# Optimization experiments

Hardware: AMD Instinct MI355X
Metric: run time of the kernel (lower is better)

Reference implementation:

```python
import jax, jax.numpy as jnp
import numpy as np

DIM = 768
NUM_HEADS = 12
HEAD_DIM = DIM // NUM_HEADS
EPS = 1e-5


def setup_inputs() -> dict:
    key = jax.random.key(0)
    ks = jax.random.split(key, 9)
    s = 1.0 / np.sqrt(DIM)
    x = jax.random.normal(ks[0], (8, 1024, DIM), dtype=jnp.float32)
    Wq = jax.random.uniform(ks[1], (DIM, DIM), jnp.float32, -s, s)
    bq = jax.random.uniform(ks[2], (DIM,), jnp.float32, -s, s)
    Wk = jax.random.uniform(ks[3], (DIM, DIM), jnp.float32, -s, s)
    bk = jax.random.uniform(ks[4], (DIM,), jnp.float32, -s, s)
    Wv = jax.random.uniform(ks[5], (DIM, DIM), jnp.float32, -s, s)
    bv = jax.random.uniform(ks[6], (DIM,), jnp.float32, -s, s)
    Wo = jax.random.uniform(ks[7], (DIM, DIM), jnp.float32, -s, s)
    bo = jax.random.uniform(ks[8], (DIM,), jnp.float32, -s, s)
    ln_g = jnp.ones((DIM,), jnp.float32)
    ln_b = jnp.zeros((DIM,), jnp.float32)
    return {"x": x, "Wq": Wq, "bq": bq, "Wk": Wk, "bk": bk, "Wv": Wv,
            "bv": bv, "Wo": Wo, "bo": bo, "ln_g": ln_g, "ln_b": ln_b}


def _layernorm(h, g, b):
    mu = jnp.mean(h, axis=-1, keepdims=True)
    var = jnp.mean(jnp.square(h - mu), axis=-1, keepdims=True)
    return (h - mu) * jax.lax.rsqrt(var + EPS) * g + b


def reference(x, Wq, bq, Wk, bk, Wv, bv, Wo, bo, ln_g, ln_b):
    B, N, C = x.shape
    H, D = NUM_HEADS, HEAD_DIM
    scaling = D ** -0.5
    q = (x @ Wq.T + bq) * scaling          # [B,N,C]
    k = x @ Wk.T + bk
    v = x @ Wv.T + bv
    q = q.reshape(B, N, H, D).transpose(0, 2, 1, 3)  # [B,H,N,D]
    k = k.reshape(B, N, H, D).transpose(0, 2, 1, 3)
    v = v.reshape(B, N, H, D).transpose(0, 2, 1, 3)
    scores = jnp.einsum('bhnd,bhmd->bhnm', q, k)     # [B,H,N,N]
    probs = jax.nn.softmax(scores.astype(jnp.float32), axis=-1).astype(scores.dtype)
    attn = jnp.einsum('bhnm,bhmd->bhnd', probs, v)   # [B,H,N,D]
    attn = attn.transpose(0, 2, 1, 3).reshape(B, N, C)
    attn = _layernorm(attn, ln_g, ln_b)
    return attn @ Wo.T + bo
```

## Files before the change

kernel.cpp:

```cpp
#include <hip/hip_runtime.h>
#include <hip/hip_bf16.h>
#include <stdint.h>


using short8  = __attribute__((ext_vector_type(8))) short;
using short4v = __attribute__((ext_vector_type(4))) short;
using floatx4 = __attribute__((ext_vector_type(4))) float;

#define LOG2E 1.44269504088896340736f

typedef __attribute__((address_space(3))) uint32_t lds_u32;
typedef const __attribute__((address_space(1))) uint32_t glb_u32;
__device__ __forceinline__ void async_copy16(const void* g, void* l) {
  __builtin_amdgcn_global_load_lds((glb_u32*)g, (lds_u32*)l, 16, 0, 0);
}

__device__ __forceinline__ float b2f(int s) {
  return __builtin_bit_cast(float, (uint32_t)((uint16_t)s) << 16);
}
__device__ __forceinline__ short f2b(float f) {
  uint32_t u = __builtin_bit_cast(uint32_t, f);
  u += 0x7fffu + ((u >> 16) & 1u);
  return (short)(u >> 16);
}
__device__ __forceinline__ uint32_t pk2(float a, float b) {
#if defined(__has_builtin) && __has_builtin(__builtin_amdgcn_cvt_pk_bf16_f32)
  typedef __bf16 bf16x2 __attribute__((ext_vector_type(2)));
  return __builtin_bit_cast(uint32_t, __builtin_amdgcn_cvt_pk_bf16_f32(a, b));
#else
  return (uint32_t)(uint16_t)f2b(a) | ((uint32_t)(uint16_t)f2b(b) << 16);
#endif
}
__device__ __forceinline__ float fexp2(float x) {
#if defined(__has_builtin) && __has_builtin(__builtin_amdgcn_exp2f)
  return __builtin_amdgcn_exp2f(x);
#else
  return exp2f(x);
#endif
}
__device__ __forceinline__ float loadf(const void* p, int idx, bool f32) {
  return f32 ? ((const float*)p)[idx] : b2f(((const short*)p)[idx]);
}
__device__ __forceinline__ short8 load8f(const void* p, int idx) {
  const float* q = (const float*)p + idx;
  float4 x0 = *(const float4*)q, x1 = *(const float4*)(q + 4);
  short8 v = {f2b(x0.x), f2b(x0.y), f2b(x0.z), f2b(x0.w),
              f2b(x1.x), f2b(x1.y), f2b(x1.z), f2b(x1.w)};
  return v;
}

__global__ __launch_bounds__(256) void cvt1_k(
    const void* __restrict__ x, const void* __restrict__ wq,
    const void* __restrict__ wk, const void* __restrict__ wv,
    const void* __restrict__ bq, const void* __restrict__ bk,
    const void* __restrict__ bv, short* __restrict__ xb,
    short* __restrict__ wqkvb, short* __restrict__ bqkvb,
    const unsigned short* __restrict__ probe) {
  if (probe[0] == 0x3F80u) return;
  int idx = blockIdx.x * 256 + threadIdx.x;
  if (idx < 786432) { *(short8*)&xb[idx * 8] = load8f(x, idx * 8); return; }
  idx -= 786432;
  if (idx < 73728) { *(short8*)&wqkvb[idx * 8] = load8f(wq, idx * 8); return; }
  idx -= 73728;
  if (idx < 73728) { *(short8*)&wqkvb[589824 + idx * 8] = load8f(wk, idx * 8); return; }
  idx -= 73728;
  if (idx < 73728) { *(short8*)&wqkvb[1179648 + idx * 8] = load8f(wv, idx * 8); return; }
  idx -= 73728;
  if (idx < 96) { *(short8*)&bqkvb[idx * 8] = load8f(bq, idx * 8); return; }
  idx -= 96;
  if (idx < 96) { *(short8*)&bqkvb[768 + idx * 8] = load8f(bk, idx * 8); return; }
  idx -= 96;
  if (idx < 96) { *(short8*)&bqkvb[1536 + idx * 8] = load8f(bv, idx * 8); return; }
}

__device__ __forceinline__ void gemm_core(const short* __restrict__ Ab,
                                          const short* __restrict__ Bb,
                                          short (*sA)[4096], short (*sB)[4096],
                                          floatx4 (&acc)[4][4]) {
  const int t = threadIdx.x;
  const int w = t >> 6, l = t & 63;
  const int lrow = l & 15, quad = l >> 4;
  const int rw = (w >> 1) * 64, cw = (w & 1) * 64;
  const int ci0 = t, ci1 = 256 + t;
  const int row0 = ci0 >> 2, ch0 = (ci0 & 3) ^ ((ci0 >> 3) & 3);
  const int row1 = ci1 >> 2, ch1 = (ci1 & 3) ^ ((ci1 >> 3) & 3);
  const short* a0 = Ab + row0 * 768 + ch0 * 8;
  const short* b0 = Bb + row0 * 768 + ch0 * 8;
  const short* a1 = Ab + row1 * 768 + ch1 * 8;
  const short* b1 = Bb + row1 * 768 + ch1 * 8;
  const int ssel = (quad ^ ((lrow >> 1) & 3)) * 8;

#define STAGE(BUF, K0)                                      \
  async_copy16(a0 + (K0), (char*)sA[BUF] + ci0 * 16);       \
  async_copy16(b0 + (K0), (char*)sB[BUF] + ci0 * 16);       \
  async_copy16(a1 + (K0), (char*)sA[BUF] + ci1 * 16);       \
  async_copy16(b1 + (K0), (char*)sB[BUF] + ci1 * 16);

  STAGE(0, 0)
  STAGE(1, 32)

#pragma unroll
  for (int it = 0; it < 24; it++) {
    if (it < 23) { asm volatile("s_waitcnt vmcnt(4)" ::: "memory"); }
    else         { asm volatile("s_waitcnt vmcnt(0)" ::: "memory"); }
    __builtin_amdgcn_s_barrier();
    asm volatile("" ::: "memory");
    __builtin_amdgcn_sched_barrier(0);
    if (it + 2 < 24) {
      STAGE((it + 2) % 3, (it + 2) * 32)
    }
    const int cur = it % 3;
    short8 af[4], bf[4];
#pragma unroll
    for (int i = 0; i < 4; i++)
      af[i] = *(const short8*)&sA[cur][(rw + i * 16 + lrow) * 32 + ssel];
#pragma unroll
    for (int j = 0; j < 4; j++)
      bf[j] = *(const short8*)&sB[cur][(cw + j * 16 + lrow) * 32 + ssel];
#pragma unroll
    for (int i = 0; i < 4; i++)
#pragma unroll
      for (int j = 0; j < 4; j++)
        acc[i][j] =
            __builtin_amdgcn_mfma_f32_16x16x32_bf16(af[i], bf[j], acc[i][j], 0, 0, 0);
  }
#undef STAGE
}

__global__ __launch_bounds__(256, 3) void gemm_qkv_k(
    const void* __restrict__ x, const short* __restrict__ xb,
    const void* __restrict__ Wq, const void* __restrict__ Wk,
    const void* __restrict__ Wv, const short* __restrict__ wqkvb,
    const void* __restrict__ bq, const void* __restrict__ bk,
    const void* __restrict__ bv, const short* __restrict__ bqkvb,
    short* __restrict__ qo, short* __restrict__ ko, short* __restrict__ vo,
    const unsigned short* __restrict__ probe) {
  __shared__ __align__(16) short sA[3][4096];
  __shared__ __align__(16) short sB[3][4096];
  const bool f32 = (probe[0] != 0x3F80u);
  const int atile = blockIdx.x, btile = blockIdx.y;
  const int sel = btile / 6;

  const short* Ab = (f32 ? xb : (const short*)x) + atile * 98304;
  const short* Bb;
  const short* biasb;
  if (f32) {
    Bb = wqkvb + btile * 98304;
    biasb = bqkvb + sel * 768;
  } else {
    const void* Wsel = sel == 0 ? Wq : (sel == 1 ? Wk : Wv);
    Bb = (const short*)Wsel + (btile - sel * 6) * 98304;
    biasb = (const short*)(sel == 0 ? bq : (sel == 1 ? bk : bv));
  }

  floatx4 acc[4][4] = {};
  gemm_core(Ab, Bb, sA, sB, acc);

  const int t = threadIdx.x, w = t >> 6, l = t & 63;
  const int lrow = l & 15, quad = l >> 4;
  const int rw = (w >> 1) * 64, cw = (w & 1) * 64;
  const int nbase = (btile - sel * 6) * 128;
#pragma unroll
  for (int i = 0; i < 4; i++) {
    const int ra0 = atile * 128 + rw + i * 16 + quad * 4;
    const int bidx = ra0 >> 10, n_in_b = ra0 & 1023;
#pragma unroll
    for (int j = 0; j < 4; j++) {
      const int cb = nbase + cw + j * 16 + lrow;
      const float bias = b2f(biasb[cb]);
      const int hh = cb >> 6, dd = cb & 63;
      if (sel == 2) {
        short4v pv;
#pragma unroll
        for (int r = 0; r < 4; r++) pv[r] = f2b(acc[i][j][r] + bias);
        const int n64 = n_in_b & 63;
        const int pos = ((n64 >> 2) & 3) * 8 + (n64 & 32) + ((n64 >> 4) & 1) * 4;
        *(short4v*)&vo[(bidx * 12 + hh) * 65536 + dd * 1024 + (n_in_b & ~63) + pos] = pv;
      } else {
        const int base = (bidx * 12 + hh) * 65536 + dd;
        short* dst = sel == 0 ? qo : ko;
#pragma unroll
        for (int r = 0; r < 4; r++) {
          float v = acc[i][j][r] + bias;
          if (sel == 0) v *= (0.125f * LOG2E);
          dst[base + (n_in_b + r) * 64] = f2b(v);
        }
      }
    }
  }
}

__global__ __launch_bounds__(256, 3) void gemm_out_k(
    const short* __restrict__ ln, const void* __restrict__ Wo,
    const short* __restrict__ wob, const void* __restrict__ bo,
    const short* __restrict__ bob, void* __restrict__ out,
    const unsigned short* __restrict__ probe) {
  __shared__ __align__(16) short sA[3][4096];
  __shared__ __align__(16) short sB[3][4096];
  const bool f32 = (probe[0] != 0x3F80u);
  const int atile = blockIdx.x, btile = blockIdx.y;
  const short* Ab = ln + atile * 98304;
  const short* Bb = (f32 ? wob : (const short*)Wo) + btile * 98304;
  const short* biasb = f32 ? bob : (const short*)bo;

  floatx4 acc[4][4] = {};
  gemm_core(Ab, Bb, sA, sB, acc);

  const int t = threadIdx.x, w = t >> 6, l = t & 63;
  const int lrow = l & 15, quad = l >> 4;
  const int rw = (w >> 1) * 64, cw = (w & 1) * 64;
#pragma unroll
  for (int i = 0; i < 4; i++) {
    const int ra0 = atile * 128 + rw + i * 16 + quad * 4;
#pragma unroll
    for (int j = 0; j < 4; j++) {
      const int cb = btile * 128 + cw + j * 16 + lrow;
      const float bias = b2f(biasb[cb]);
#pragma unroll
      for (int r = 0; r < 4; r++) {
        float v = acc[i][j][r] + bias;
        if (f32) ((float*)out)[(ra0 + r) * 768 + cb] = v;
        else     ((short*)out)[(ra0 + r) * 768 + cb] = f2b(v);
      }
    }
  }
}

__global__ __launch_bounds__(256, 5) void attn_k(const short* __restrict__ q,
                                                 const short* __restrict__ k,
                                                 const short* __restrict__ vt,
                                                 short* __restrict__ o) {
  __shared__ __align__(16) short sMem[2][8192];

  const int t = threadIdx.x, w = t >> 6, l = t & 63;
  const int lrow = l & 15, quad = l >> 4;
  const int bh = blockIdx.x, qt = blockIdx.y;
  const int b = bh / 12, h = bh % 12;
  const short* qb = q + bh * 65536 + qt * 4096;
  const short* kb = k + bh * 65536;
  const short* vb = vt + bh * 65536;

  const int srow = t >> 3, sgc = (t & 7) ^ (srow & 7);
  const short* kst = kb + srow * 64 + sgc * 8;
  const short* vst = vb + srow * 1024 + sgc * 8;

  const int swz0 = (quad ^ (lrow & 7)) * 16;
  const int swz1 = ((4 + quad) ^ (lrow & 7)) * 16;
  const char* s0 = (const char*)&sMem[0][0];
  const char* kp0 = s0 + lrow * 128 + swz0;
  const char* kp1 = s0 + lrow * 128 + swz1;
  const char* vp0 = s0 + 8192 + lrow * 128 + swz0;
  const char* vp1 = s0 + 8192 + lrow * 128 + swz1;

#pragma unroll
  for (int i = 0; i < 2; i++) {
    const int ci = i * 256 + t;
    const int row = ci >> 3, gc = (ci & 7) ^ (row & 7);
    async_copy16(qb + row * 64 + gc * 8, (char*)sMem[1] + ci * 16);
  }
  async_copy16(kst, (char*)sMem[0] + t * 16);
  async_copy16(kst + 2048, (char*)sMem[0] + 4096 + t * 16);
  async_copy16(vst, (char*)sMem[0] + 8192 + t * 16);
  async_copy16(vst + 32768, (char*)sMem[0] + 12288 + t * 16);
  __syncthreads();

  short8 qf[2];
  const int qr = w * 16 + lrow;
#pragma unroll
  for (int dc = 0; dc < 2; dc++)
    qf[dc] = *(const short8*)&sMem[1][qr * 64 + ((dc * 4 + quad) ^ (qr & 7)) * 8];
  __syncthreads();

  const short one_b = (short)0x3F80;
  const short8 ones8 = {one_b, one_b, one_b, one_b, one_b, one_b, one_b, one_b};
  floatx4 l_acc = {};
  floatx4 o_acc[4] = {};

#define ATTN_BODY(CUR, IT)                                                     \
  {                                                                            \
    if ((IT) < 15) {                                                           \
      const int nxt = (CUR) ^ 1;                                               \
      const short* ksrc = kst + ((IT) + 1) * 4096;                             \
      const short* vsrc = vst + ((IT) + 1) * 64;                               \
      async_copy16(ksrc, (char*)sMem[nxt] + t * 16);                           \
      async_copy16(ksrc + 2048, (char*)sMem[nxt] + 4096 + t * 16);             \
      async_copy16(vsrc, (char*)sMem[nxt] + 8192 + t * 16);                    \
      async_copy16(vsrc + 32768, (char*)sMem[nxt] + 12288 + t * 16);           \
    }                                                                          \
    short4v pf[4];                                                             \
    _Pragma("unroll")                                                          \
    for (int g = 0; g < 4; g++) {                                              \
      short8 kf0 = *(const short8*)(kp0 + (CUR) * 16384 + g * 2048);           \
      short8 kf1 = *(const short8*)(kp1 + (CUR) * 16384 + g * 2048);           \
      floatx4 st = {};                                                         \
      st = __builtin_amdgcn_mfma_f32_16x16x32_bf16(kf0, qf[0], st, 0, 0, 0);   \
      st = __builtin_amdgcn_mfma_f32_16x16x32_bf16(kf1, qf[1], st, 0, 0, 0);   \
      uint2 pp = {pk2(fexp2(st[0]), fexp2(st[1])),                             \
                  pk2(fexp2(st[2]), fexp2(st[3]))};                            \
      pf[g] = __builtin_bit_cast(short4v, pp);                                 \
    }                                                                          \
    const short8 pa0 =                                                         \
        __builtin_shufflevector(pf[0], pf[1], 0, 1, 2, 3, 4, 5, 6, 7);         \
    const short8 pa1 =                                                         \
        __builtin_shufflevector(pf[2], pf[3], 0, 1, 2, 3, 4, 5, 6, 7);         \
    l_acc = __builtin_amdgcn_mfma_f32_16x16x32_bf16(pa0, ones8, l_acc, 0, 0, 0); \
    l_acc = __builtin_amdgcn_mfma_f32_16x16x32_bf16(pa1, ones8, l_acc, 0, 0, 0); \
    _Pragma("unroll")                                                          \
    for (int j2 = 0; j2 < 4; j2++) {                                           \
      short8 vv0 = *(const short8*)(vp0 + (CUR) * 16384 + j2 * 2048);          \
      short8 vv1 = *(const short8*)(vp1 + (CUR) * 16384 + j2 * 2048);          \
      o_acc[j2] =                                                              \
          __builtin_amdgcn_mfma_f32_16x16x32_bf16(pa0, vv0, o_acc[j2], 0, 0, 0); \
      o_acc[j2] =                                                              \
          __builtin_amdgcn_mfma_f32_16x16x32_bf16(pa1, vv1, o_acc[j2], 0, 0, 0); \
    }                                                                          \
    __syncthreads();                                                           \
  }

  for (int it2 = 0; it2 < 8; it2++) {
    ATTN_BODY(0, it2 * 2)
    ATTN_BODY(1, it2 * 2 + 1)
  }
#undef ATTN_BODY

  float inv_l[4];
#pragma unroll
  for (int r = 0; r < 4; r++) inv_l[r] = 1.0f / l_acc[r];
  const int n0 = qt * 64 + w * 16 + quad * 4;
#pragma unroll
  for (int j2 = 0; j2 < 4; j2++) {
    const int d = j2 * 16 + lrow;
#pragma unroll
    for (int r = 0; r < 4; r++)
      o[(b * 1024 + n0 + r) * 768 + h * 64 + d] = f2b(o_acc[j2][r] * inv_l[r]);
  }
}

__global__ __launch_bounds__(256) void lncvt_k(const short* __restrict__ in,
                                               const void* __restrict__ g,
                                               const void* __restrict__ be,
                                               short* __restrict__ out,
                                               const void* __restrict__ wo,
                                               const void* __restrict__ bo,
                                               short* __restrict__ wob,
                                               short* __restrict__ bob,
                                               const unsigned short* __restrict__ probe) {
  const bool f32 = (probe[0] != 0x3F80u);
  if (blockIdx.x >= 2048) {
    if (!f32) return;
    int idx = (blockIdx.x - 2048) * 256 + threadIdx.x;
    if (idx < 73728) { *(short8*)&wob[idx * 8] = load8f(wo, idx * 8); return; }
    idx -= 73728;
    if (idx < 96) { *(short8*)&bob[idx * 8] = load8f(bo, idx * 8); }
    return;
  }
  const int w = threadIdx.x >> 6, l = threadIdx.x & 63;
  const int row = blockIdx.x * 4 + w;
  const short* rp = in + row * 768;
  float v[12];
  float s = 0.f, ss = 0.f;
#pragma unroll
  for (int c = 0; c < 3; c++) {
    ushort4 u = *(const ushort4*)&rp[(c * 64 + l) * 4];
    float f0 = b2f(u.x), f1 = b2f(u.y), f2 = b2f(u.z), f3 = b2f(u.w);
    v[c * 4 + 0] = f0; v[c * 4 + 1] = f1; v[c * 4 + 2] = f2; v[c * 4 + 3] = f3;
    s += (f0 + f1) + (f2 + f3);
    ss += (f0 * f0 + f1 * f1) + (f2 * f2 + f3 * f3);
  }
#pragma unroll
  for (int msk = 1; msk < 64; msk <<= 1) {
    s += __shfl_xor(s, msk);
    ss += __shfl_xor(ss, msk);
  }
  const float mu = s * (1.f / 768.f);
  const float rstd = rsqrtf(ss * (1.f / 768.f) - mu * mu + 1e-5f);
  short* op = out + row * 768;
#pragma unroll
  for (int c = 0; c < 3; c++) {
    const int base = (c * 64 + l) * 4;
    ushort4 r;
    r.x = (unsigned short)(unsigned)f2b((v[c * 4 + 0] - mu) * rstd * loadf(g, base + 0, f32) + loadf(be, base + 0, f32));
    r.y = (unsigned short)(unsigned)f2b((v[c * 4 + 1] - mu) * rstd * loadf(g, base + 1, f32) + loadf(be, base + 1, f32));
    r.z = (unsigned short)(unsigned)f2b((v[c * 4 + 2] - mu) * rstd * loadf(g, base + 2, f32) + loadf(be, base + 2, f32));
    r.w = (unsigned short)(unsigned)f2b((v[c * 4 + 3] - mu) * rstd * loadf(g, base + 3, f32) + loadf(be, base + 3, f32));
    *(ushort4*)&op[base] = r;
  }
}

extern "C" void kernel_launch(void* const* d_in, const int* in_sizes, int n_in,
                              void* d_out, int out_size, void* d_ws, size_t ws_size,
                              hipStream_t stream) {
  const void* x    = d_in[0];
  const void* Wq   = d_in[1];
  const void* bq   = d_in[2];
  const void* Wk   = d_in[3];
  const void* bk   = d_in[4];
  const void* Wv   = d_in[5];
  const void* bv   = d_in[6];
  const void* Wo   = d_in[7];
  const void* bo   = d_in[8];
  const void* ln_g = d_in[9];
  const void* ln_b = d_in[10];
  const unsigned short* probe = (const unsigned short*)d_in[9];

  char* ws = (char*)d_ws;
  const size_t SZ = 12582912;
  if (ws_size < 3 * SZ) return;
  short* qbuf = (short*)ws;
  short* kbuf = (short*)(ws + SZ);
  short* vtb  = (short*)(ws + 2 * SZ);

  char* outc = (char*)d_out;
  short* wqkvb = (short*)outc;
  short* bqkvb = (short*)(outc + 3538944);
  short* xb    = (short*)(outc + 12582912);
  short* wob   = (short*)(ws + SZ);
  short* bob   = (short*)(ws + SZ + 1179648);

  dim3 blk(256);
  cvt1_k<<<3938, blk, 0, stream>>>(x, Wq, Wk, Wv, bq, bk, bv, xb, wqkvb, bqkvb, probe);
  gemm_qkv_k<<<dim3(64, 18), blk, 0, stream>>>(x, xb, Wq, Wk, Wv, wqkvb, bq, bk, bv,
                                               bqkvb, qbuf, kbuf, vtb, probe);
  attn_k<<<dim3(96, 16), blk, 0, stream>>>(qbuf, kbuf, vtb, (short*)d_out);
  lncvt_k<<<2337, blk, 0, stream>>>((short*)d_out, ln_g, ln_b, qbuf,
                                    Wo, bo, wob, bob, probe);
  gemm_out_k<<<dim3(64, 6), blk, 0, stream>>>(qbuf, Wo, wob, bo, bob, d_out, probe);
}
```

Baseline: 217.8 us.

## Widen QKV GEMM tile to 128x192 with double-buffered LDS

The QKV projection GEMM now uses 128x192 output tiles instead of 128x128. Each wave holds a 4x6 MFMA accumulator block, and the grid shrinks from 64x18 to 64x12 blocks. The LDS pipeline drops from three buffers to two, with a full wait and barrier each k-step. The wider tile raises arithmetic intensity and cuts A-tile reloads. The cost is more accumulator registers, fewer blocks (768, which may under-fill the CUs) and a shallower prefetch pipeline.

```diff
diff --git a/kernel.cpp b/kernel.cpp
--- a/kernel.cpp
+++ b/kernel.cpp
@@ -73,6 +73,59 @@
   if (idx < 96) { *(short8*)&bqkvb[1536 + idx * 8] = load8f(bv, idx * 8); return; }
 }
 
+__device__ __forceinline__ void gemm_core192(const short* __restrict__ Ab,
+                                             const short* __restrict__ Bb,
+                                             short (*sA)[4096], short (*sB)[6144],
+                                             floatx4 (&acc)[4][6]) {
+  const int t = threadIdx.x;
+  const int w = t >> 6, l = t & 63;
+  const int lrow = l & 15, quad = l >> 4;
+  const int rw = (w >> 1) * 64, cw = (w & 1) * 96;
+  const int ac0 = t, ac1 = 256 + t;
+  const int bc0 = t, bc1 = 256 + t, bc2 = 512 + t;
+  const short* a0 = Ab + (ac0 >> 2) * 768 + ((ac0 & 3) ^ ((ac0 >> 3) & 3)) * 8;
+  const short* a1 = Ab + (ac1 >> 2) * 768 + ((ac1 & 3) ^ ((ac1 >> 3) & 3)) * 8;
+  const short* b0 = Bb + (bc0 >> 2) * 768 + ((bc0 & 3) ^ ((bc0 >> 3) & 3)) * 8;
+  const short* b1 = Bb + (bc1 >> 2) * 768 + ((bc1 & 3) ^ ((bc1 >> 3) & 3)) * 8;
+  const short* b2 = Bb + (bc2 >> 2) * 768 + ((bc2 & 3) ^ ((bc2 >> 3) & 3)) * 8;
+  const int ssel = (quad ^ ((lrow >> 1) & 3)) * 8;
+
+#define STAGE192(BUF, K0)                                   \
+  async_copy16(a0 + (K0), (char*)sA[BUF] + ac0 * 16);       \
+  async_copy16(a1 + (K0), (char*)sA[BUF] + ac1 * 16);       \
+  async_copy16(b0 + (K0), (char*)sB[BUF] + bc0 * 16);       \
+  async_copy16(b1 + (K0), (char*)sB[BUF] + bc1 * 16);       \
+  async_copy16(b2 + (K0), (char*)sB[BUF] + bc2 * 16);
+
+  STAGE192(0, 0)
+
+#pragma unroll
+  for (int it = 0; it < 24; it++) {
+    asm volatile("s_waitcnt vmcnt(0)" ::: "memory");
+    __builtin_amdgcn_s_barrier();
+    asm volatile("" ::: "memory");
+    __builtin_amdgcn_sched_barrier(0);
+    if (it < 23) {
+      STAGE192((it + 1) & 1, (it + 1) * 32)
+    }
+    const int cur = it & 1;
+    short8 af[4], bf[6];
+#pragma unroll
+    for (int i = 0; i < 4; i++)
+      af[i] = *(const short8*)&sA[cur][(rw + i * 16 + lrow) * 32 + ssel];
+#pragma unroll
+    for (int j = 0; j < 6; j++)
+      bf[j] = *(const short8*)&sB[cur][(cw + j * 16 + lrow) * 32 + ssel];
+#pragma unroll
+    for (int i = 0; i < 4; i++)
+#pragma unroll
+      for (int j = 0; j < 6; j++)
+        acc[i][j] =
+            __builtin_amdgcn_mfma_f32_16x16x32_bf16(af[i], bf[j], acc[i][j], 0, 0, 0);
+  }
+#undef STAGE192
+}
+
 __device__ __forceinline__ void gemm_core(const short* __restrict__ Ab,
                                           const short* __restrict__ Bb,
                                           short (*sA)[4096], short (*sB)[4096],
@@ -135,37 +188,37 @@
     const void* __restrict__ bv, const short* __restrict__ bqkvb,
     short* __restrict__ qo, short* __restrict__ ko, short* __restrict__ vo,
     const unsigned short* __restrict__ probe) {
-  __shared__ __align__(16) short sA[3][4096];
-  __shared__ __align__(16) short sB[3][4096];
+  __shared__ __align__(16) short sA[2][4096];
+  __shared__ __align__(16) short sB[2][6144];
   const bool f32 = (probe[0] != 0x3F80u);
   const int atile = blockIdx.x, btile = blockIdx.y;
-  const int sel = btile / 6;
+  const int sel = btile >> 2;
 
   const short* Ab = (f32 ? xb : (const short*)x) + atile * 98304;
   const short* Bb;
   const short* biasb;
   if (f32) {
-    Bb = wqkvb + btile * 98304;
+    Bb = wqkvb + btile * 147456;
     biasb = bqkvb + sel * 768;
   } else {
     const void* Wsel = sel == 0 ? Wq : (sel == 1 ? Wk : Wv);
-    Bb = (const short*)Wsel + (btile - sel * 6) * 98304;
+    Bb = (const short*)Wsel + (btile - sel * 4) * 147456;
     biasb = (const short*)(sel == 0 ? bq : (sel == 1 ? bk : bv));
   }
 
-  floatx4 acc[4][4] = {};
-  gemm_core(Ab, Bb, sA, sB, acc);
+  floatx4 acc[4][6] = {};
+  gemm_core192(Ab, Bb, sA, sB, acc);
 
   const int t = threadIdx.x, w = t >> 6, l = t & 63;
   const int lrow = l & 15, quad = l >> 4;
-  const int rw = (w >> 1) * 64, cw = (w & 1) * 64;
-  const int nbase = (btile - sel * 6) * 128;
+  const int rw = (w >> 1) * 64, cw = (w & 1) * 96;
+  const int nbase = (btile - sel * 4) * 192;
 #pragma unroll
   for (int i = 0; i < 4; i++) {
     const int ra0 = atile * 128 + rw + i * 16 + quad * 4;
     const int bidx = ra0 >> 10, n_in_b = ra0 & 1023;
 #pragma unroll
-    for (int j = 0; j < 4; j++) {
+    for (int j = 0; j < 6; j++) {
       const int cb = nbase + cw + j * 16 + lrow;
       const float bias = b2f(biasb[cb]);
       const int hh = cb >> 6, dd = cb & 63;
@@ -419,7 +472,7 @@
 
   dim3 blk(256);
   cvt1_k<<<3938, blk, 0, stream>>>(x, Wq, Wk, Wv, bq, bk, bv, xb, wqkvb, bqkvb, probe);
-  gemm_qkv_k<<<dim3(64, 18), blk, 0, stream>>>(x, xb, Wq, Wk, Wv, wqkvb, bq, bk, bv,
+  gemm_qkv_k<<<dim3(64, 12), blk, 0, stream>>>(x, xb, Wq, Wk, Wv, wqkvb, bq, bk, bv,
                                                bqkvb, qbuf, kbuf, vtb, probe);
   attn_k<<<dim3(96, 16), blk, 0, stream>>>(qbuf, kbuf, vtb, (short*)d_out);
   lncvt_k<<<2337, blk, 0, stream>>>((short*)d_out, ln_g, ln_b, qbuf,
```

After: 215.3 us, median of 2. About the same (-1.2%).
